# Optimization experiments

Hardware: AMD Instinct MI355X
Metric: run time of the kernel (lower is better)

The kernel has to match this reference:

```python
import jax, jax.numpy as jnp
import numpy as np

LAMB = 1.0
EPS = 1e-16


def setup_inputs() -> dict:
    key = jax.random.key(0)
    kx, km = jax.random.split(key)
    N, D, K = 262144, 128, 64
    x = jax.random.normal(kx, (N, D), dtype=jnp.float32)
    m = jax.random.normal(km, (K, D), dtype=jnp.float32)
    m = m / jnp.linalg.norm(m, axis=1, keepdims=True)  # unit-norm rows like __init__
    return {"x": x, "m": m}


def _entropy(p):
    # replicate torch.where clamping
    p = jnp.where(p <= 0, EPS, p)
    p = jnp.where(p >= 1, 1.0 - EPS, p)
    return -jnp.sum(p * jnp.log(p), axis=-1)


def _p(x, m):
    d2 = (jnp.sum(x * x, axis=-1, keepdims=True)
          - 2.0 * x @ m.T
          + jnp.sum(m * m, axis=-1))  # [N, K]
    return jax.nn.softmax(-d2, axis=-1)


def reference(x, m):
    p = _p(x, m)                      # [N, K]
    intra = jnp.mean(_entropy(p))     # scalar
    mu = jnp.mean(m, axis=0)          # [D]
    p_inter = _p(mu[None, :], m)[0]   # [K]
    inter = _entropy(p_inter)
    total = intra - LAMB * inter
    return (total, intra, inter)
```

## Files before the change

kernel.cpp:

```cpp
#include <hip/hip_runtime.h>

#define D 128
#define K 64

typedef __attribute__((ext_vector_type(8))) short short8;
typedef __attribute__((ext_vector_type(4))) short bf4;
typedef __attribute__((ext_vector_type(4))) float f32x4;

__device__ inline short f2bf(float f) {
  union { float f; unsigned u; } v; v.f = f;
  unsigned u = v.u;
  return (short)((u + 0x7fffu + ((u >> 16) & 1u)) >> 16);
}

template<int CTRL>
__device__ inline float dpp_ror(float x) {
  return __builtin_bit_cast(float, __builtin_amdgcn_update_dpp(
      0, __builtin_bit_cast(int, x), CTRL, 0xF, 0xF, true));
}
__device__ inline float rowsum16(float v) {
  v += dpp_ror<0x121>(v);
  v += dpp_ror<0x122>(v);
  v += dpp_ror<0x124>(v);
  v += dpp_ror<0x128>(v);
  return v;
}
__device__ inline float rowmax16(float v) {
  v = fmaxf(v, dpp_ror<0x121>(v));
  v = fmaxf(v, dpp_ror<0x122>(v));
  v = fmaxf(v, dpp_ror<0x124>(v));
  v = fmaxf(v, dpp_ror<0x128>(v));
  return v;
}

__global__ void prep_kernel(const float* __restrict__ m, float* ws) {
  int tid = threadIdx.x;
  if (tid < 16) ws[tid] = 0.0f;
  if (tid < K) {
    const float* mr = m + tid * D;
    float s = 0.f;
    for (int d = 0; d < D; ++d) s += mr[d] * mr[d];
    ws[16 + tid] = s;
  }
  short* mb = (short*)(ws + 128);
  for (int i = tid; i < K * D; i += blockDim.x) mb[i] = f2bf(2.0f * m[i]);
}

__launch_bounds__(256, 4)
__global__ void main_kernel(const float* __restrict__ x, float* ws, int nTiles, int totalWaves) {
  __shared__ short8 bsm[1024];
  __shared__ char asmem[4][4096];

  const float* mnorm = ws + 16;
  const short8* mbv = (const short8*)(ws + 128);
  for (int i = threadIdx.x; i < 1024; i += blockDim.x)
    bsm[i ^ ((i >> 4) & 7)] = mbv[i];
  __syncthreads();

  const int lane = threadIdx.x & 63;
  const int lid  = lane & 15;
  const int quad = lane >> 4;
  const int wid  = threadIdx.x >> 6;
  char* amem = asmem[wid];

  float mn[4];
#pragma unroll
  for (int jt = 0; jt < 4; ++jt) mn[jt] = mnorm[jt * 16 + lid];

  int cbase[4];
#pragma unroll
  for (int kk = 0; kk < 4; ++kk)
    cbase[kk] = (lid * 16 + kk * 4 + quad) ^ (lid & 7);

  const int hi = lane >> 5;
  const int wc = (lane & 31) >> 1;
  const int wh = lane & 1;

  int ra[4];
#pragma unroll
  for (int kk = 0; kk < 4; ++kk)
    ra[kk] = lid * 256 + ((((kk << 2) | quad) ^ lid) << 4);

  const int wave = blockIdx.x * (blockDim.x >> 6) + wid;
  float hacc = 0.f;

  f32x4 ld[8];
  {
    const float* xb = x + (size_t)wave * (16 * D) + lane * 4;
#pragma unroll
    for (int p = 0; p < 8; ++p) ld[p] = *(const f32x4*)(xb + p * 256);
  }

  for (int t = wave; t < nTiles; t += totalWaves) {
#pragma unroll
    for (int p = 0; p < 8; ++p) {
      f32x4 v = ld[p];
      bf4 s;
      s[0] = f2bf(v[0]); s[1] = f2bf(v[1]); s[2] = f2bf(v[2]); s[3] = f2bf(v[3]);
      int r = 2 * p + hi;
      *(bf4*)(amem + r * 256 + ((wc ^ r) << 4) + wh * 8) = s;
    }

    int tn = t + totalWaves;
    if (tn < nTiles) {
      const float* xb = x + (size_t)tn * (16 * D) + lane * 4;
#pragma unroll
      for (int p = 0; p < 8; ++p) ld[p] = *(const f32x4*)(xb + p * 256);
    }

    short8 a[4];
#pragma unroll
    for (int kk = 0; kk < 4; ++kk)
      a[kk] = *(const short8*)(amem + ra[kk]);

    f32x4 acc[4];
#pragma unroll
    for (int jt = 0; jt < 4; ++jt) acc[jt] = (f32x4){0.f, 0.f, 0.f, 0.f};
#pragma unroll
    for (int kk = 0; kk < 4; ++kk)
#pragma unroll
      for (int jt = 0; jt < 4; ++jt) {
        short8 b = bsm[cbase[kk] + jt * 256];
        acc[jt] = __builtin_amdgcn_mfma_f32_16x16x32_bf16(a[kk], b, acc[jt], 0, 0, 0);
      }

#pragma unroll
    for (int r = 0; r < 4; ++r) {
      float s0 = acc[0][r] - mn[0];
      float s1 = acc[1][r] - mn[1];
      float s2 = acc[2][r] - mn[2];
      float s3 = acc[3][r] - mn[3];
      float mx = rowmax16(fmaxf(fmaxf(s0, s1), fmaxf(s2, s3)));
      float t0 = s0 - mx, t1 = s1 - mx, t2 = s2 - mx, t3 = s3 - mx;
      float e0 = __expf(t0), e1 = __expf(t1), e2 = __expf(t2), e3 = __expf(t3);
      float S0 = rowsum16((e0 + e1) + (e2 + e3));
      float S1 = rowsum16((t0 * e0 + t1 * e1) + (t2 * e2 + t3 * e3));
      float H = __logf(S0) - S1 / S0;
      if (lid == 0) hacc += H;
    }
  }

  for (int off = 1; off < 64; off <<= 1) hacc += __shfl_xor(hacc, off, 64);
  __shared__ float red[4];
  if (lane == 0) red[wid] = hacc;
  __syncthreads();
  if (threadIdx.x == 0) atomicAdd(ws, red[0] + red[1] + red[2] + red[3]);
}

__global__ void final_kernel(const float* __restrict__ m, const float* ws, float* out, int nRows) {
  __shared__ float mu[D];
  int lane = threadIdx.x;
  for (int d = lane; d < D; d += 64) {
    float s = 0.f;
    for (int j = 0; j < K; ++j) s += m[j * D + d];
    mu[d] = s * (1.0f / K);
  }
  __syncthreads();
  const float* mr = m + lane * D;
  float dot = 0.f;
  for (int d = 0; d < D; ++d) dot += mu[d] * mr[d];
  float s = 2.f * dot - ws[16 + lane];
  float mx = s;
  for (int off = 1; off < 64; off <<= 1) mx = fmaxf(mx, __shfl_xor(mx, off, 64));
  float t = s - mx;
  float e = __expf(t);
  float S0 = e, S1 = t * e;
  for (int off = 1; off < 64; off <<= 1) {
    S0 += __shfl_xor(S0, off, 64);
    S1 += __shfl_xor(S1, off, 64);
  }
  float inter = __logf(S0) - S1 / S0;
  if (lane == 0) {
    float intra = ws[0] / (float)nRows;
    out[0] = intra - inter;
    out[1] = intra;
    out[2] = inter;
  }
}

extern "C" void kernel_launch(void* const* d_in, const int* in_sizes, int n_in,
                              void* d_out, int out_size, void* d_ws, size_t ws_size,
                              hipStream_t stream) {
  const float* x = (const float*)d_in[0];
  const float* m = (const float*)d_in[1];
  float* ws = (float*)d_ws;
  float* out = (float*)d_out;
  const int N = in_sizes[0] / D;
  const int nTiles = N / 16;

  prep_kernel<<<1, 256, 0, stream>>>(m, ws);

  const int blocks = 1024;
  const int totalWaves = blocks * 4;
  main_kernel<<<blocks, 256, 0, stream>>>(x, ws, nTiles, totalWaves);

  final_kernel<<<1, 64, 0, stream>>>(m, ws, out, N);
}
```

Before: 215.2 us.

## Fuse prep into main kernel, double-buffer x loads, use packed bf16 convert

Removes the single-block prep kernel: each block now converts m to bf16 into shared memory and computes row norms itself, and the workspace accumulator is cleared with a memset. The main loop keeps two register buffers of x tiles in flight, so each load has a full tile of compute to hide behind. The bf16 conversion uses the hardware packed convert instruction instead of manual rounding. In exchange, every block redundantly reads m and computes norms, and the extra buffers raise register pressure, which could cut occupancy.

```diff
diff --git a/kernel.cpp b/kernel.cpp
--- a/kernel.cpp
+++ b/kernel.cpp
@@ -4,13 +4,19 @@
 #define K 64
 
 typedef __attribute__((ext_vector_type(8))) short short8;
-typedef __attribute__((ext_vector_type(4))) short bf4;
+typedef __attribute__((ext_vector_type(2))) int int2v;
 typedef __attribute__((ext_vector_type(4))) float f32x4;
 
 __device__ inline short f2bf(float f) {
   union { float f; unsigned u; } v; v.f = f;
   unsigned u = v.u;
   return (short)((u + 0x7fffu + ((u >> 16) & 1u)) >> 16);
+}
+
+__device__ inline int cvt_pk_bf16(float lo, float hi) {
+  int r;
+  asm("v_cvt_pk_bf16_f32 %0, %1, %2" : "=v"(r) : "v"(lo), "v"(hi));
+  return r;
 }
 
 template<int CTRL>
@@ -33,118 +39,121 @@
   return v;
 }
 
-__global__ void prep_kernel(const float* __restrict__ m, float* ws) {
-  int tid = threadIdx.x;
-  if (tid < 16) ws[tid] = 0.0f;
+#define LOADX(dst, t) do {                                                  \
+    const f32x4* xb = (const f32x4*)(x + (size_t)(t) * (16 * D)) + lane;    \
+    _Pragma("unroll") for (int p = 0; p < 8; ++p) dst[p] = xb[p * 64];      \
+  } while (0)
+
+#define PACKX(src) do {                                                     \
+    _Pragma("unroll") for (int p = 0; p < 8; ++p) {                         \
+      f32x4 v = src[p];                                                     \
+      int2v s;                                                              \
+      s[0] = cvt_pk_bf16(v[0], v[1]);                                       \
+      s[1] = cvt_pk_bf16(v[2], v[3]);                                       \
+      int r = 2 * p + hi;                                                   \
+      *(int2v*)(amem + r * 256 + ((wc ^ r) << 4) + wh * 8) = s;             \
+    }                                                                       \
+  } while (0)
+
+#define TILE_COMPUTE() do {                                                 \
+    f32x4 acc[4];                                                           \
+    _Pragma("unroll") for (int jt = 0; jt < 4; ++jt)                        \
+      acc[jt] = (f32x4){0.f, 0.f, 0.f, 0.f};                                \
+    _Pragma("unroll") for (int kk = 0; kk < 4; ++kk) {                      \
+      short8 afrag = *(const short8*)(amem + ra[kk]);                       \
+      _Pragma("unroll") for (int jt = 0; jt < 4; ++jt)                      \
+        acc[jt] = __builtin_amdgcn_mfma_f32_16x16x32_bf16(                  \
+            afrag, bsm[cbase[kk] + jt * 256], acc[jt], 0, 0, 0);            \
+    }                                                                       \
+    _Pragma("unroll") for (int r = 0; r < 4; ++r) {                         \
+      float s0 = acc[0][r] - mn[0];                                         \
+      float s1 = acc[1][r] - mn[1];                                         \
+      float s2 = acc[2][r] - mn[2];                                         \
+      float s3 = acc[3][r] - mn[3];                                         \
+      float mx = rowmax16(fmaxf(fmaxf(s0, s1), fmaxf(s2, s3)));             \
+      float t0 = s0 - mx, t1 = s1 - mx, t2 = s2 - mx, t3 = s3 - mx;         \
+      float e0 = __expf(t0), e1 = __expf(t1);                               \
+      float e2 = __expf(t2), e3 = __expf(t3);                               \
+      float S0 = rowsum16((e0 + e1) + (e2 + e3));                           \
+      float S1 = rowsum16((t0 * e0 + t1 * e1) + (t2 * e2 + t3 * e3));       \
+      float H = __logf(S0) - S1 / S0;                                       \
+      hacc += (lid == 0) ? H : 0.0f;                                        \
+    }                                                                       \
+  } while (0)
+
+__launch_bounds__(256, 4)
+__global__ void main_kernel(const float* __restrict__ x, const float* __restrict__ m,
+                            float* ws, int nTiles, int totalWaves) {
+  __shared__ short8 bsm[1024];
+  __shared__ float mnorms[K];
+  __shared__ char asmem[4][4096];
+
+  const int tid = threadIdx.x;
+  for (int i = tid; i < K * D; i += 256) {
+    int c = i >> 3, e = i & 7;
+    int cs = c ^ ((c >> 4) & 7);
+    ((short*)bsm)[cs * 8 + e] = f2bf(2.0f * m[i]);
+  }
   if (tid < K) {
     const float* mr = m + tid * D;
     float s = 0.f;
     for (int d = 0; d < D; ++d) s += mr[d] * mr[d];
-    ws[16 + tid] = s;
-  }
-  short* mb = (short*)(ws + 128);
-  for (int i = tid; i < K * D; i += blockDim.x) mb[i] = f2bf(2.0f * m[i]);
-}
-
-__launch_bounds__(256, 4)
-__global__ void main_kernel(const float* __restrict__ x, float* ws, int nTiles, int totalWaves) {
-  __shared__ short8 bsm[1024];
-  __shared__ char asmem[4][4096];
-
-  const float* mnorm = ws + 16;
-  const short8* mbv = (const short8*)(ws + 128);
-  for (int i = threadIdx.x; i < 1024; i += blockDim.x)
-    bsm[i ^ ((i >> 4) & 7)] = mbv[i];
+    mnorms[tid] = s;
+  }
   __syncthreads();
 
-  const int lane = threadIdx.x & 63;
+  const int lane = tid & 63;
   const int lid  = lane & 15;
   const int quad = lane >> 4;
-  const int wid  = threadIdx.x >> 6;
+  const int wid  = tid >> 6;
   char* amem = asmem[wid];
 
   float mn[4];
 #pragma unroll
-  for (int jt = 0; jt < 4; ++jt) mn[jt] = mnorm[jt * 16 + lid];
-
-  int cbase[4];
+  for (int jt = 0; jt < 4; ++jt) mn[jt] = mnorms[jt * 16 + lid];
+
+  int cbase[4], ra[4];
 #pragma unroll
-  for (int kk = 0; kk < 4; ++kk)
+  for (int kk = 0; kk < 4; ++kk) {
     cbase[kk] = (lid * 16 + kk * 4 + quad) ^ (lid & 7);
+    ra[kk] = lid * 256 + ((((kk << 2) | quad) ^ lid) << 4);
+  }
 
   const int hi = lane >> 5;
   const int wc = (lane & 31) >> 1;
   const int wh = lane & 1;
 
-  int ra[4];
-#pragma unroll
-  for (int kk = 0; kk < 4; ++kk)
-    ra[kk] = lid * 256 + ((((kk << 2) | quad) ^ lid) << 4);
-
-  const int wave = blockIdx.x * (blockDim.x >> 6) + wid;
+  const int wave = blockIdx.x * 4 + wid;
+  const int step = 2 * totalWaves;
   float hacc = 0.f;
 
-  f32x4 ld[8];
-  {
-    const float* xb = x + (size_t)wave * (16 * D) + lane * 4;
-#pragma unroll
-    for (int p = 0; p < 8; ++p) ld[p] = *(const f32x4*)(xb + p * 256);
-  }
-
-  for (int t = wave; t < nTiles; t += totalWaves) {
-#pragma unroll
-    for (int p = 0; p < 8; ++p) {
-      f32x4 v = ld[p];
-      bf4 s;
-      s[0] = f2bf(v[0]); s[1] = f2bf(v[1]); s[2] = f2bf(v[2]); s[3] = f2bf(v[3]);
-      int r = 2 * p + hi;
-      *(bf4*)(amem + r * 256 + ((wc ^ r) << 4) + wh * 8) = s;
-    }
-
-    int tn = t + totalWaves;
-    if (tn < nTiles) {
-      const float* xb = x + (size_t)tn * (16 * D) + lane * 4;
-#pragma unroll
-      for (int p = 0; p < 8; ++p) ld[p] = *(const f32x4*)(xb + p * 256);
-    }
-
-    short8 a[4];
-#pragma unroll
-    for (int kk = 0; kk < 4; ++kk)
-      a[kk] = *(const short8*)(amem + ra[kk]);
-
-    f32x4 acc[4];
-#pragma unroll
-    for (int jt = 0; jt < 4; ++jt) acc[jt] = (f32x4){0.f, 0.f, 0.f, 0.f};
-#pragma unroll
-    for (int kk = 0; kk < 4; ++kk)
-#pragma unroll
-      for (int jt = 0; jt < 4; ++jt) {
-        short8 b = bsm[cbase[kk] + jt * 256];
-        acc[jt] = __builtin_amdgcn_mfma_f32_16x16x32_bf16(a[kk], b, acc[jt], 0, 0, 0);
-      }
-
-#pragma unroll
-    for (int r = 0; r < 4; ++r) {
-      float s0 = acc[0][r] - mn[0];
-      float s1 = acc[1][r] - mn[1];
-      float s2 = acc[2][r] - mn[2];
-      float s3 = acc[3][r] - mn[3];
-      float mx = rowmax16(fmaxf(fmaxf(s0, s1), fmaxf(s2, s3)));
-      float t0 = s0 - mx, t1 = s1 - mx, t2 = s2 - mx, t3 = s3 - mx;
-      float e0 = __expf(t0), e1 = __expf(t1), e2 = __expf(t2), e3 = __expf(t3);
-      float S0 = rowsum16((e0 + e1) + (e2 + e3));
-      float S1 = rowsum16((t0 * e0 + t1 * e1) + (t2 * e2 + t3 * e3));
-      float H = __logf(S0) - S1 / S0;
-      if (lid == 0) hacc += H;
-    }
+  f32x4 ldA[8], ldB[8];
+  int tA = wave, tB = wave + totalWaves;
+  const int iters = nTiles / step;
+  if (tA < nTiles) LOADX(ldA, tA);
+  if (tB < nTiles) LOADX(ldB, tB);
+
+  for (int it = 0; it < iters; ++it) {
+    const bool more = (it + 1 < iters);
+    PACKX(ldA);
+    if (more) LOADX(ldA, tA + step);
+    TILE_COMPUTE();
+    PACKX(ldB);
+    if (more) LOADX(ldB, tB + step);
+    TILE_COMPUTE();
+    tA += step; tB += step;
+  }
+  for (int t = wave + iters * step; t < nTiles; t += totalWaves) {
+    LOADX(ldA, t);
+    PACKX(ldA);
+    TILE_COMPUTE();
   }
 
   for (int off = 1; off < 64; off <<= 1) hacc += __shfl_xor(hacc, off, 64);
   __shared__ float red[4];
   if (lane == 0) red[wid] = hacc;
   __syncthreads();
-  if (threadIdx.x == 0) atomicAdd(ws, red[0] + red[1] + red[2] + red[3]);
+  if (tid == 0) atomicAdd(ws, red[0] + red[1] + red[2] + red[3]);
 }
 
 __global__ void final_kernel(const float* __restrict__ m, const float* ws, float* out, int nRows) {
@@ -157,9 +166,12 @@
   }
   __syncthreads();
   const float* mr = m + lane * D;
-  float dot = 0.f;
-  for (int d = 0; d < D; ++d) dot += mu[d] * mr[d];
-  float s = 2.f * dot - ws[16 + lane];
+  float dot = 0.f, nrm = 0.f;
+  for (int d = 0; d < D; ++d) {
+    dot += mu[d] * mr[d];
+    nrm += mr[d] * mr[d];
+  }
+  float s = 2.f * dot - nrm;
   float mx = s;
   for (int off = 1; off < 64; off <<= 1) mx = fmaxf(mx, __shfl_xor(mx, off, 64));
   float t = s - mx;
@@ -188,11 +200,11 @@
   const int N = in_sizes[0] / D;
   const int nTiles = N / 16;
 
-  prep_kernel<<<1, 256, 0, stream>>>(m, ws);
+  hipMemsetAsync(ws, 0, 64, stream);
 
   const int blocks = 1024;
   const int totalWaves = blocks * 4;
-  main_kernel<<<blocks, 256, 0, stream>>>(x, ws, nTiles, totalWaves);
+  main_kernel<<<blocks, 256, 0, stream>>>(x, m, ws, nTiles, totalWaves);
 
   final_kernel<<<1, 64, 0, stream>>>(m, ws, out, N);
 }
```

Measured after the change: 204.8 us. -4.8%, faster.
